# Performance work log

Hardware: AMD Instinct MI355X
Metric: run time of the kernel (lower is better)

The kernel has to match this reference:

```python
import jax, jax.numpy as jnp
import numpy as np

B, A, D, K = 128, 64, 256, 2048


def setup_inputs() -> dict:
    key = jax.random.key(0)
    k1, k2, k3, k4 = jax.random.split(key, 4)
    return {
        "continuous_latent": jax.random.normal(k1, (B, A, D), dtype=jnp.float32),
        "codebook": jax.random.normal(k2, (K, D), dtype=jnp.float32),
        "codebook_weights": jax.random.uniform(k3, (K,), dtype=jnp.float32),
        "rand_idx": jax.random.randint(k4, (K,), 0, B * A, dtype=jnp.int64)
        if jax.config.jax_enable_x64 else jax.random.randint(k4, (K,), 0, B * A, dtype=jnp.int32),
    }


def reference(continuous_latent, codebook, codebook_weights, rand_idx):
    b, a, d = continuous_latent.shape
    k = codebook.shape[0]
    sg = jax.lax.stop_gradient

    # (same math as the torch broadcast-subtract-square-sum, but avoids the
    # (B, A, K, D) intermediate by using a GEMM)
    x_sq = jnp.sum(continuous_latent * continuous_latent, axis=-1, keepdims=True)  # (B, A, 1)
    c_sq = jnp.sum(codebook * codebook, axis=-1)                                   # (K,)
    xc = jnp.einsum("bad,kd->bak", continuous_latent, codebook)                    # (B, A, K)
    distances = x_sq + c_sq[None, None, :] - 2.0 * xc                              # (B, A, K)

    soft_one_hot = jax.nn.softmax(-100.0 * distances, axis=-1)  # (B, A, K)

    args_selected = jnp.argmin(distances, axis=-1)  # (B, A)
    quantized = codebook[args_selected]             # (B, A, D)

    # Uselessness: pull rarely-used codes toward random encoder outputs.
    random_latents = continuous_latent.reshape(b * a, d)[rand_idx]  # (K, D)
    total_samples = jnp.sum(codebook_weights)
    unused = codebook_weights < total_samples / (100.0 * k)         # (K,)
    diff = jnp.where(unused[:, None], sg(random_latents) - codebook,
                     jnp.zeros_like(codebook))
    uselessness = jnp.mean(jnp.sum(jnp.log(jnp.abs(diff) + 1.0), axis=-1))

    quantization_loss = jnp.mean(
        jnp.sum((continuous_latent - quantized) ** 2, axis=-1))

    # Straight-through estimator
    quantized_ste = sg(quantized) + continuous_latent - sg(continuous_latent)

    # Latent diversity: mean over (B, B, A) of ||x_i,a - x_j,a||^2, computed
    # via the norm expansion to avoid the (B, B, A, D) intermediate.
    n = jnp.sum(continuous_latent * continuous_latent, axis=-1)         # (B, A)
    inner = jnp.einsum("iad,jad->ija", continuous_latent, continuous_latent)
    latent_diversity = jnp.mean(n[:, None, :] + n[None, :, :] - 2.0 * inner)

    probs = jnp.ones_like(quantized_ste[..., 0]) / k  # (B, A)

    return (quantized_ste, probs, soft_one_hot,
            quantization_loss, uselessness, latent_diversity)
```

## Files before the change

### kernel.cpp

```cpp
#include <hip/hip_runtime.h>

#define B_ 128
#define A_ 64
#define D_ 256
#define K_ 2048
#define R_ (B_*A_)
#define KEFF 512
#define QB 32

typedef __attribute__((ext_vector_type(8))) short bf16x8;
typedef __attribute__((ext_vector_type(4))) float f32x4;

__device__ inline float waveReduceSum(float v) {
    #pragma unroll
    for (int off = 32; off > 0; off >>= 1)
        v += __shfl_xor(v, off, 64);
    return v;
}
__device__ inline unsigned short f2bf(float f) {
    unsigned int u = __float_as_uint(f);
    return (unsigned short)((u + 0x7fffu + ((u >> 16) & 1u)) >> 16);
}
__device__ inline float bf2f(unsigned short h) {
    return __uint_as_float((unsigned int)h << 16);
}
__device__ inline bool ltidx(float a, int ia, float b, int ib) {
    return a < b || (a == b && ia < ib);
}

__global__ __launch_bounds__(256) void prologue_kernel(
        const float* __restrict__ X, const float* __restrict__ C,
        const float* __restrict__ W, const int* __restrict__ ridx,
        short* __restrict__ XPs, short* __restrict__ CP1s,
        float* __restrict__ xsq, float* __restrict__ csq,
        float* __restrict__ cspart, double* __restrict__ acc) {
    int bid = blockIdx.x;
    int wave = threadIdx.x >> 6, lane = threadIdx.x & 63;
    if (bid < 2048) {
        int row = bid * 4 + wave;
        int korig = lane * 4;
        float4 v = *reinterpret_cast<const float4*>(X + (size_t)row * D_ + korig);
        float f[4] = {v.x, v.y, v.z, v.w};
        ushort4 hi, lo;
        unsigned short* hp = (unsigned short*)&hi;
        unsigned short* lp = (unsigned short*)&lo;
        float s = 0.f;
        #pragma unroll
        for (int q = 0; q < 4; ++q) {
            s += f[q] * f[q];
            unsigned short h = f2bf(f[q]);
            hp[q] = h;
            lp[q] = f2bf(f[q] - bf2f(h));
        }
        int S = row >> 5, r32 = row & 31;
        int t = korig >> 5, kc = (korig >> 3) & 3, j = korig & 7;
        size_t base = (size_t)S * 16384 + (size_t)kc * 256 + (size_t)r32 * 8 + j;
        *reinterpret_cast<ushort4*>(XPs + base + (size_t)t * 1024)       = hi;
        *reinterpret_cast<ushort4*>(XPs + base + (size_t)(t + 8) * 1024) = lo;
        s = waveReduceSum(s);
        if (lane == 0) xsq[row] = s;
    } else if (bid < 2560) {
        int row = (bid - 2048) * 4 + wave;
        int korig = lane * 4;
        float4 v = *reinterpret_cast<const float4*>(C + (size_t)row * D_ + korig);
        float f[4] = {v.x, v.y, v.z, v.w};
        ushort4 hi, lo;
        unsigned short* hp = (unsigned short*)&hi;
        unsigned short* lp = (unsigned short*)&lo;
        float s = 0.f;
        #pragma unroll
        for (int q = 0; q < 4; ++q) {
            s += f[q] * f[q];
            unsigned short h = f2bf(f[q]);
            hp[q] = h;
            lp[q] = f2bf(f[q] - bf2f(h));
        }
        int rb = row >> 7, r = row & 127;
        int t = korig >> 5, kc = (korig >> 3) & 3, j = korig & 7;
        size_t base = ((size_t)rb * 16) * 4096 + (size_t)kc * 1024 + (size_t)r * 8 + j;
        *reinterpret_cast<ushort4*>(CP1s + base + (size_t)t * 4096)       = hi;
        *reinterpret_cast<ushort4*>(CP1s + base + (size_t)(t + 8) * 4096) = lo;
        s = waveReduceSum(s);
        if (lane == 0) csq[row] = s;
    } else if (bid < 2624) {
        int idx = (bid - 2560) * 256 + threadIdx.x;
        float s = 0.f;
        #pragma unroll 4
        for (int i = 0; i < B_; ++i) s += X[(size_t)i * (A_*D_) + idx];
        float p = s * s;
        p = waveReduceSum(p);
        __shared__ float red[4];
        if (lane == 0) red[wave] = p;
        __syncthreads();
        if (threadIdx.x == 0) cspart[bid - 2560] = red[0] + red[1] + red[2] + red[3];
    } else {
        double s = 0.0;
        for (int i = threadIdx.x; i < K_; i += 256) s += (double)W[i];
        __shared__ double red[256];
        red[threadIdx.x] = s; __syncthreads();
        for (int off = 128; off > 0; off >>= 1) {
            if (threadIdx.x < off) red[threadIdx.x] += red[threadIdx.x + off];
            __syncthreads();
        }
        float cutoff = (float)(red[0] / (100.0 * (double)K_));
        int k = (bid - 2624) * 4 + wave;
        if (!(W[k] < cutoff)) return;
        int r = ridx[k];
        float4 xv = *reinterpret_cast<const float4*>(X + (size_t)r * D_ + lane * 4);
        float4 cv = *reinterpret_cast<const float4*>(C + (size_t)k * D_ + lane * 4);
        float u = logf(fabsf(xv.x - cv.x) + 1.f) + logf(fabsf(xv.y - cv.y) + 1.f)
                + logf(fabsf(xv.z - cv.z) + 1.f) + logf(fabsf(xv.w - cv.w) + 1.f);
        u = waveReduceSum(u);
        if (lane == 0) atomicAdd(acc + 3, (double)u);
    }
}

__global__ __launch_bounds__(512, 2) void fused_dist_softmax(
        const short* __restrict__ XPs, const short* __restrict__ CP1s,
        const float* __restrict__ xsq, const float* __restrict__ csq,
        const float* __restrict__ X, const float* __restrict__ C,
        float* __restrict__ soft, float* __restrict__ outq,
        float* __restrict__ probs, float* __restrict__ qlrow) {
    __shared__ short ALDS[16384];
    __shared__ float csl[K_];
    __shared__ float xls[QB];
    __shared__ float4 wtop[8][QB];
    __shared__ float wsuml[8][QB];
    __shared__ float4 ffin[QB];
    __shared__ float finv[QB];

    int tid = threadIdx.x;
    int lane = tid & 63, w = tid >> 6;
    int S = blockIdx.x;
    int kc = lane >> 4, lr = lane & 15;

    #pragma unroll
    for (int p = 0; p < 4; ++p) {
        int seg0 = p * 16 + w * 2;
        const short* gsrc = XPs + (size_t)S * 16384
                          + (size_t)(seg0 + (lane >> 5)) * 256 + (lane & 31) * 8;
        short* ldst = &ALDS[seg0 * 256];
        __builtin_amdgcn_global_load_lds(
            (const __attribute__((address_space(1))) unsigned int*)gsrc,
            (__attribute__((address_space(3))) unsigned int*)ldst, 16, 0, 0);
    }
    *reinterpret_cast<float4*>(&csl[tid * 4]) =
        *reinterpret_cast<const float4*>(csq + tid * 4);
    if (tid < QB) xls[tid] = xsq[S * QB + tid];
    __syncthreads();

    f32x4 acc[2][16] = {};

    for (int tau = 0; tau < 16; ++tau) {
        const int ta = tau & 7;
        bf16x8 a1[2], a2[2];
        #pragma unroll
        for (int rt = 0; rt < 2; ++rt) {
            a1[rt] = *(const bf16x8*)(&ALDS[((ta * 4 + kc) * 32 + rt * 16 + lr) * 8]);
            a2[rt] = *(const bf16x8*)(&ALDS[(((ta + 8) * 4 + kc) * 32 + rt * 16 + lr) * 8]);
        }
        #pragma unroll
        for (int g = 0; g < 4; ++g) {
            const int cb = w * 2 + (g >> 1);
            const short* bbase = CP1s + ((size_t)(cb * 16 + tau)) * 4096
                               + (size_t)kc * 1024 + (size_t)lr * 8
                               + (size_t)((g & 1) * 4) * 128;
            bf16x8 bfr[4];
            #pragma unroll
            for (int c4 = 0; c4 < 4; ++c4)
                bfr[c4] = *(const bf16x8*)(bbase + c4 * 128);
            #pragma unroll
            for (int c4 = 0; c4 < 4; ++c4) {
                const int ct = g * 4 + c4;
                #pragma unroll
                for (int rt = 0; rt < 2; ++rt) {
                    acc[rt][ct] = __builtin_amdgcn_mfma_f32_16x16x32_bf16(bfr[c4], a1[rt], acc[rt][ct], 0, 0, 0);
                    acc[rt][ct] = __builtin_amdgcn_mfma_f32_16x16x32_bf16(bfr[c4], a2[rt], acc[rt][ct], 0, 0, 0);
                }
            }
        }
    }

    const float4* csl4 = reinterpret_cast<const float4*>(csl);

    #pragma unroll
    for (int rt = 0; rt < 2; ++rt) {
        int row32 = rt * 16 + lr;
        float xs = xls[row32];
        float bv1 = 3.4e38f, bv2 = 3.4e38f;
        int bi1 = 0x7fffffff, bi2 = 0x7fffffff;
        #pragma unroll
        for (int ct = 0; ct < 16; ++ct) {
            int col0 = w * 256 + ct * 16 + kc * 4;
            float4 cs = csl4[col0 >> 2];
            float csa[4] = {cs.x, cs.y, cs.z, cs.w};
            #pragma unroll
            for (int j = 0; j < 4; ++j) {
                float d = fmaf(-2.f, acc[rt][ct][j], xs + csa[j]);
                int idx = col0 + j;
                if (d < bv1) { bv2 = bv1; bi2 = bi1; bv1 = d; bi1 = idx; }
                else if (ltidx(d, idx, bv2, bi2)) { bv2 = d; bi2 = idx; }
            }
        }
        #pragma unroll
        for (int off = 16; off <= 32; off <<= 1) {
            float o1 = __shfl_xor(bv1, off, 64); int oi1 = __shfl_xor(bi1, off, 64);
            float o2 = __shfl_xor(bv2, off, 64); int oi2 = __shfl_xor(bi2, off, 64);
            if (ltidx(o1, oi1, bv1, bi1)) {
                if (ltidx(bv1, bi1, o2, oi2)) { bv2 = bv1; bi2 = bi1; }
                else                          { bv2 = o2;  bi2 = oi2; }
                bv1 = o1; bi1 = oi1;
            } else if (ltidx(o1, oi1, bv2, bi2)) { bv2 = o1; bi2 = oi1; }
        }
        if (kc == 0)
            wtop[w][row32] = make_float4(bv1, __int_as_float(bi1),
                                         bv2, __int_as_float(bi2));
    }
    __syncthreads();

    if (tid < QB) {
        float4 m = wtop[0][tid];
        float f1 = m.x; int a1i = __float_as_int(m.y);
        float f2 = m.z; int a2i = __float_as_int(m.w);
        #pragma unroll
        for (int ww = 1; ww < 8; ++ww) {
            float4 q = wtop[ww][tid];
            float o1 = q.x; int oi1 = __float_as_int(q.y);
            float o2 = q.z; int oi2 = __float_as_int(q.w);
            if (ltidx(o1, oi1, f1, a1i)) {
                if (ltidx(f1, a1i, o2, oi2)) { f2 = f1; a2i = a1i; }
                else                         { f2 = o2; a2i = oi2; }
                f1 = o1; a1i = oi1;
            } else if (ltidx(o1, oi1, f2, a2i)) { f2 = o1; a2i = oi1; }
        }
        ffin[tid] = make_float4(f1, __int_as_float(a1i), f2, __int_as_float(a2i));
    }
    __syncthreads();

    #pragma unroll
    for (int rt = 0; rt < 2; ++rt) {
        int row32 = rt * 16 + lr;
        float xs = xls[row32];
        float dm = ffin[row32].x;
        float psum = 0.f;
        #pragma unroll
        for (int ct = 0; ct < 16; ++ct) {
            int col0 = w * 256 + ct * 16 + kc * 4;
            float4 cs = csl4[col0 >> 2];
            float csa[4] = {cs.x, cs.y, cs.z, cs.w};
            #pragma unroll
            for (int j = 0; j < 4; ++j) {
                float d = fmaf(-2.f, acc[rt][ct][j], xs + csa[j]);
                float e = __expf(-100.f * (d - dm));
                acc[rt][ct][j] = e;
                psum += e;
            }
        }
        #pragma unroll
        for (int off = 16; off <= 32; off <<= 1) psum += __shfl_xor(psum, off, 64);
        if (kc == 0) wsuml[w][row32] = psum;
    }
    __syncthreads();
    if (tid < QB) {
        float s = 0.f;
        #pragma unroll
        for (int ww = 0; ww < 8; ++ww) s += wsuml[ww][tid];
        finv[tid] = 1.f / s;
    }
    __syncthreads();

    size_t rowbase = (size_t)S * QB;
    #pragma unroll
    for (int rt = 0; rt < 2; ++rt) {
        int row32 = rt * 16 + lr;
        float inv = finv[row32];
        float* dst0 = soft + (rowbase + row32) * K_ + w * 256 + kc * 4;
        #pragma unroll
        for (int ct = 0; ct < 16; ++ct) {
            f32x4 o = acc[rt][ct] * inv;
            *reinterpret_cast<f32x4*>(dst0 + ct * 16) = o;
        }
    }

    #pragma unroll
    for (int i = 0; i < 4; ++i) {
        int row32 = w * 4 + i;
        size_t grow = rowbase + row32;
        float4 fm = ffin[row32];
        int am = __float_as_int(fm.y), am2 = __float_as_int(fm.w);
        float4 x  = *reinterpret_cast<const float4*>(X + grow * D_ + lane * 4);
        float4 c1 = *reinterpret_cast<const float4*>(C + (size_t)am  * D_ + lane * 4);
        float4 c2 = *reinterpret_cast<const float4*>(C + (size_t)am2 * D_ + lane * 4);
        float d1 = (x.x-c1.x)*(x.x-c1.x) + (x.y-c1.y)*(x.y-c1.y)
                 + (x.z-c1.z)*(x.z-c1.z) + (x.w-c1.w)*(x.w-c1.w);
        float d2 = (x.x-c2.x)*(x.x-c2.x) + (x.y-c2.y)*(x.y-c2.y)
                 + (x.z-c2.z)*(x.z-c2.z) + (x.w-c2.w)*(x.w-c2.w);
        d1 = waveReduceSum(d1);
        d2 = waveReduceSum(d2);
        bool p2 = ltidx(d2, am2, d1, am);
        float4 q = p2 ? c2 : c1;
        *reinterpret_cast<float4*>(outq + grow * D_ + lane * 4) = q;
        if (lane == 0) {
            qlrow[grow] = p2 ? d2 : d1;
            probs[grow] = 1.0f / (float)K_;
        }
    }
}

__global__ void row_sqnorm(const float* __restrict__ X, float* __restrict__ out, int rows) {
    int wave = threadIdx.x >> 6, lane = threadIdx.x & 63;
    int row  = blockIdx.x * 4 + wave;
    if (row >= rows) return;
    float4 v = *reinterpret_cast<const float4*>(X + (size_t)row * D_ + lane * 4);
    float s = v.x*v.x + v.y*v.y + v.z*v.z + v.w*v.w;
    s = waveReduceSum(s);
    if (lane == 0) out[row] = s;
}

__global__ void col_sum_sq(const float* __restrict__ X, float* __restrict__ part) {
    int idx = blockIdx.x * blockDim.x + threadIdx.x;
    float s = 0.f;
    #pragma unroll 4
    for (int i = 0; i < B_; ++i) s += X[(size_t)i * (A_*D_) + idx];
    float p = s * s;
    p = waveReduceSum(p);
    __shared__ float red[4];
    int wave = threadIdx.x >> 6, lane = threadIdx.x & 63;
    if (lane == 0) red[wave] = p;
    __syncthreads();
    if (threadIdx.x == 0) part[blockIdx.x] = red[0] + red[1] + red[2] + red[3];
}

__global__ void wsum_kernel(const float* __restrict__ w, double* __restrict__ acc) {
    double s = 0.0;
    for (int i = threadIdx.x; i < K_; i += 256) s += (double)w[i];
    __shared__ double red[256];
    red[threadIdx.x] = s; __syncthreads();
    for (int off = 128; off > 0; off >>= 1) {
        if (threadIdx.x < off) red[threadIdx.x] += red[threadIdx.x + off];
        __syncthreads();
    }
    if (threadIdx.x == 0) acc[2] = red[0];
}

__global__ void useless_kernel(const float* __restrict__ X, const float* __restrict__ C,
                               const float* __restrict__ w, const int* __restrict__ ridx,
                               const double* __restrict__ acc_in, double* __restrict__ use_acc) {
    int wave = threadIdx.x >> 6, lane = threadIdx.x & 63;
    int k = blockIdx.x * 4 + wave;
    if (k >= K_) return;
    float cutoff = (float)(acc_in[2] / (100.0 * (double)K_));
    if (!(w[k] < cutoff)) return;
    int r = ridx[k];
    float4 xv = *reinterpret_cast<const float4*>(X + (size_t)r * D_ + lane * 4);
    float4 cv = *reinterpret_cast<const float4*>(C + (size_t)k * D_ + lane * 4);
    float s = logf(fabsf(xv.x - cv.x) + 1.f) + logf(fabsf(xv.y - cv.y) + 1.f)
            + logf(fabsf(xv.z - cv.z) + 1.f) + logf(fabsf(xv.w - cv.w) + 1.f);
    s = waveReduceSum(s);
    if (lane == 0) atomicAdd(use_acc, (double)s);
}

#define BM 128
#define BN 128
#define BK 16
__global__ __launch_bounds__(256, 4) void dist_gemm(
        const float* __restrict__ X, const float* __restrict__ C,
        const float* __restrict__ xsq, const float* __restrict__ csq,
        float* __restrict__ Dist) {
    __shared__ float As[BK][BM + 4];
    __shared__ float Bs[BK][BN + 4];
    int tid = threadIdx.x;
    int tx = tid & 15, ty = tid >> 4;
    int bm0 = blockIdx.y * BM, bn0 = blockIdx.x * BN;
    int r = tid & 127;
    const float* src = (tid < 128) ? (X + (size_t)(bm0 + r) * D_)
                                   : (C + (size_t)(bn0 + r) * D_);
    float* dst = (tid < 128) ? &As[0][0] : &Bs[0][0];
    float acc[2][2][4][4] = {};
    float4 p0 = *reinterpret_cast<const float4*>(src + 0);
    float4 p1 = *reinterpret_cast<const float4*>(src + 4);
    float4 p2 = *reinterpret_cast<const float4*>(src + 8);
    float4 p3 = *reinterpret_cast<const float4*>(src + 12);
    for (int t = 0; t < D_ / BK; ++t) {
        __syncthreads();
        dst[ 0*(BM+4) + r] = p0.x; dst[ 1*(BM+4) + r] = p0.y;
        dst[ 2*(BM+4) + r] = p0.z; dst[ 3*(BM+4) + r] = p0.w;
        dst[ 4*(BM+4) + r] = p1.x; dst[ 5*(BM+4) + r] = p1.y;
        dst[ 6*(BM+4) + r] = p1.z; dst[ 7*(BM+4) + r] = p1.w;
        dst[ 8*(BM+4) + r] = p2.x; dst[ 9*(BM+4) + r] = p2.y;
        dst[10*(BM+4) + r] = p2.z; dst[11*(BM+4) + r] = p2.w;
        dst[12*(BM+4) + r] = p3.x; dst[13*(BM+4) + r] = p3.y;
        dst[14*(BM+4) + r] = p3.z; dst[15*(BM+4) + r] = p3.w;
        __syncthreads();
        if (t < D_ / BK - 1) {
            const float* s2 = src + (t + 1) * BK;
            p0 = *reinterpret_cast<const float4*>(s2 + 0);
            p1 = *reinterpret_cast<const float4*>(s2 + 4);
            p2 = *reinterpret_cast<const float4*>(s2 + 8);
            p3 = *reinterpret_cast<const float4*>(s2 + 12);
        }
        #pragma unroll
        for (int kk = 0; kk < BK; ++kk) {
            float4 a0 = *reinterpret_cast<const float4*>(&As[kk][ty * 4]);
            float4 a1 = *reinterpret_cast<const float4*>(&As[kk][64 + ty * 4]);
            float4 b0 = *reinterpret_cast<const float4*>(&Bs[kk][tx * 4]);
            float4 b1 = *reinterpret_cast<const float4*>(&Bs[kk][64 + tx * 4]);
            float af[2][4] = {{a0.x, a0.y, a0.z, a0.w}, {a1.x, a1.y, a1.z, a1.w}};
            float bf[2][4] = {{b0.x, b0.y, b0.z, b0.w}, {b1.x, b1.y, b1.z, b1.w}};
            #pragma unroll
            for (int rg = 0; rg < 2; ++rg)
                #pragma unroll
                for (int cg = 0; cg < 2; ++cg)
                    #pragma unroll
                    for (int i = 0; i < 4; ++i)
                        #pragma unroll
                        for (int j = 0; j < 4; ++j)
                            acc[rg][cg][i][j] += af[rg][i] * bf[cg][j];
        }
    }
    #pragma unroll
    for (int rg = 0; rg < 2; ++rg)
        #pragma unroll
        for (int i = 0; i < 4; ++i) {
            int row = bm0 + rg * 64 + ty * 4 + i;
            float xs = xsq[row];
            #pragma unroll
            for (int cg = 0; cg < 2; ++cg) {
                int col = bn0 + cg * 64 + tx * 4;
                float4 cs = *reinterpret_cast<const float4*>(csq + col);
                float4 o;
                o.x = xs + cs.x - 2.f * acc[rg][cg][i][0];
                o.y = xs + cs.y - 2.f * acc[rg][cg][i][1];
                o.z = xs + cs.z - 2.f * acc[rg][cg][i][2];
                o.w = xs + cs.w - 2.f * acc[rg][cg][i][3];
                *reinterpret_cast<float4*>(Dist + (size_t)row * K_ + col) = o;
            }
        }
}

__global__ __launch_bounds__(256) void softmax_quant(
        float* __restrict__ Dist, const float* __restrict__ X,
        const float* __restrict__ C, float* __restrict__ outq,
        float* __restrict__ probs, float* __restrict__ qlrow) {
    int row = blockIdx.x;
    int t = threadIdx.x;
    int wave = t >> 6, lane = t & 63;
    float* drow = Dist + (size_t)row * K_;

    float v[8];
    float4 v0 = *reinterpret_cast<const float4*>(drow + t * 8);
    float4 v1v = *reinterpret_cast<const float4*>(drow + t * 8 + 4);
    v[0]=v0.x; v[1]=v0.y; v[2]=v0.z; v[3]=v0.w;
    v[4]=v1v.x; v[5]=v1v.y; v[6]=v1v.z; v[7]=v1v.w;

    float v1 = v[0]; int i1 = t * 8;
    float v2 = 3.4e38f; int i2 = 0x7fffffff;
    #pragma unroll
    for (int j = 1; j < 8; ++j) {
        int idx = t * 8 + j;
        if (v[j] < v1) { v2 = v1; i2 = i1; v1 = v[j]; i1 = idx; }
        else if (ltidx(v[j], idx, v2, i2)) { v2 = v[j]; i2 = idx; }
    }
    #pragma unroll
    for (int off = 32; off > 0; off >>= 1) {
        float w1 = __shfl_xor(v1, off, 64); int j1 = __shfl_xor(i1, off, 64);
        float w2 = __shfl_xor(v2, off, 64); int j2 = __shfl_xor(i2, off, 64);
        if (ltidx(w1, j1, v1, i1)) {
            if (ltidx(v1, i1, w2, j2)) { v2 = v1; i2 = i1; }
            else                       { v2 = w2; i2 = j2; }
            v1 = w1; i1 = j1;
        } else if (ltidx(w1, j1, v2, i2)) { v2 = w1; i2 = j1; }
    }
    __shared__ float sv1[4], sv2[4]; __shared__ int si1[4], si2[4];
    __shared__ float ws[4];
    if (lane == 0) { sv1[wave] = v1; si1[wave] = i1; sv2[wave] = v2; si2[wave] = i2; }
    __syncthreads();
    float dmin = sv1[0]; int am = si1[0];
    float d2nd = sv2[0]; int am2 = si2[0];
    #pragma unroll
    for (int w = 1; w < 4; ++w) {
        float w1 = sv1[w]; int j1 = si1[w];
        float w2 = sv2[w]; int j2 = si2[w];
        if (ltidx(w1, j1, dmin, am)) {
            if (ltidx(dmin, am, w2, j2)) { d2nd = dmin; am2 = am; }
            else                         { d2nd = w2;   am2 = j2; }
            dmin = w1; am = j1;
        } else if (ltidx(w1, j1, d2nd, am2)) { d2nd = w1; am2 = j1; }
    }

    float e[8]; float s = 0.f;
    #pragma unroll
    for (int j = 0; j < 8; ++j) { e[j] = __expf(-100.f * (v[j] - dmin)); s += e[j]; }
    s = waveReduceSum(s);
    if (lane == 0) ws[wave] = s;
    __syncthreads();
    float inv = 1.f / (ws[0] + ws[1] + ws[2] + ws[3]);

    float4 o0 = make_float4(e[0]*inv, e[1]*inv, e[2]*inv, e[3]*inv);
    float4 o1 = make_float4(e[4]*inv, e[5]*inv, e[6]*inv, e[7]*inv);
    *reinterpret_cast<float4*>(drow + t * 8)     = o0;
    *reinterpret_cast<float4*>(drow + t * 8 + 4) = o1;

    if (wave == 0) {
        float4 x  = *reinterpret_cast<const float4*>(X + (size_t)row * D_ + lane * 4);
        float4 c1 = *reinterpret_cast<const float4*>(C + (size_t)am  * D_ + lane * 4);
        float4 c2 = *reinterpret_cast<const float4*>(C + (size_t)am2 * D_ + lane * 4);
        float d1x = (x.x-c1.x)*(x.x-c1.x) + (x.y-c1.y)*(x.y-c1.y)
                  + (x.z-c1.z)*(x.z-c1.z) + (x.w-c1.w)*(x.w-c1.w);
        float d2x = (x.x-c2.x)*(x.x-c2.x) + (x.y-c2.y)*(x.y-c2.y)
                  + (x.z-c2.z)*(x.z-c2.z) + (x.w-c2.w)*(x.w-c2.w);
        d1x = waveReduceSum(d1x);
        d2x = waveReduceSum(d2x);
        bool pick2 = ltidx(d2x, am2, d1x, am);
        float4 q = pick2 ? c2 : c1;
        float dq = pick2 ? d2x : d1x;
        *reinterpret_cast<float4*>(outq + (size_t)row * D_ + lane * 4) = q;
        if (lane == 0) {
            qlrow[row] = dq;
            probs[row] = 1.0f / (float)K_;
        }
    }
}

__global__ __launch_bounds__(256) void finalize_kernel(
        const double* __restrict__ acc, const float* __restrict__ xsq,
        const float* __restrict__ qlrow, const float* __restrict__ cspart,
        float* __restrict__ o) {
    int t = threadIdx.x;
    double xs = 0.0, ql = 0.0, cs = 0.0;
    for (int i = t; i < R_; i += 256) { xs += (double)xsq[i]; ql += (double)qlrow[i]; }
    if (t < 64) cs = (double)cspart[t];
    __shared__ double r0[256], r1[256], r2[256];
    r0[t] = xs; r1[t] = ql; r2[t] = cs;
    __syncthreads();
    for (int off = 128; off > 0; off >>= 1) {
        if (t < off) { r0[t] += r0[t+off]; r1[t] += r1[t+off]; r2[t] += r2[t+off]; }
        __syncthreads();
    }
    if (t == 0) {
        o[0] = (float)(r1[0] / (double)R_);
        o[1] = (float)(acc[3] / (double)K_);
        o[2] = (float)(2.0 * r0[0] / (double)R_
                     - 2.0 * r2[0] / ((double)B_ * (double)B_ * (double)A_));
    }
}

extern "C" void kernel_launch(void* const* d_in, const int* in_sizes, int n_in,
                              void* d_out, int out_size, void* d_ws, size_t ws_size,
                              hipStream_t stream) {
    const float* X  = (const float*)d_in[0];
    const float* C  = (const float*)d_in[1];
    const float* W  = (const float*)d_in[2];
    const int*   RI = (const int*)d_in[3];

    float* out    = (float*)d_out;
    float* out_q  = out;
    float* out_p  = out_q + (size_t)R_ * D_;
    float* out_s  = out_p + R_;
    float* out_sc = out_s + (size_t)R_ * K_;

    char* wsb = (char*)d_ws;
    double* acc   = (double*)wsb;
    float*  xsq   = (float*)(wsb + 64);
    float*  csq   = (float*)(wsb + 64 + R_*4);
    float*  qlrow = (float*)(wsb + 64 + R_*4 + K_*4);
    float*  cspart= (float*)(wsb + 64 + R_*4 + K_*4 + R_*4);
    short*  CP1s  = (short*)(wsb + 64 + R_*4 + K_*4 + R_*4 + 256);

    const size_t WS_NEEDED = 64 + (size_t)R_*4 + (size_t)K_*4 + (size_t)R_*4 + 256
                           + (size_t)K_*KEFF*2;

    hipMemsetAsync(d_ws, 0, 64, stream);

    if (ws_size >= WS_NEEDED) {
        short* XPs = (short*)out_q;
        hipLaunchKernelGGL(prologue_kernel, dim3(3136), dim3(256), 0, stream,
                           X, C, W, RI, XPs, CP1s, xsq, csq, cspart, acc);
        hipLaunchKernelGGL(fused_dist_softmax, dim3(R_/QB), dim3(512), 0, stream,
                           XPs, CP1s, xsq, csq, X, C, out_s, out_q, out_p, qlrow);
    } else {
        hipLaunchKernelGGL(row_sqnorm, dim3(R_/4), dim3(256), 0, stream, X, xsq, R_);
        hipLaunchKernelGGL(row_sqnorm, dim3(K_/4), dim3(256), 0, stream, C, csq, K_);
        hipLaunchKernelGGL(col_sum_sq, dim3((A_*D_)/256), dim3(256), 0, stream, X, cspart);
        hipLaunchKernelGGL(wsum_kernel, dim3(1), dim3(256), 0, stream, W, acc);
        hipLaunchKernelGGL(useless_kernel, dim3(K_/4), dim3(256), 0, stream,
                           X, C, W, RI, acc, acc + 3);
        hipLaunchKernelGGL(dist_gemm, dim3(K_/BN, R_/BM), dim3(256), 0, stream, X, C, xsq, csq, out_s);
        hipLaunchKernelGGL(softmax_quant, dim3(R_), dim3(256), 0, stream, out_s, X, C, out_q, out_p, qlrow);
    }

    hipLaunchKernelGGL(finalize_kernel, dim3(1), dim3(256), 0, stream, acc, xsq, qlrow, cspart, out_sc);
}
```

Before: 89.70 us.

## Fuse X bf16 hi/lo split and row norms into the distance kernel

Moves the conversion of X into split bf16 hi/lo fragments, and its row-norm computation, from the prologue kernel into the fused distance/softmax kernel. Each block now writes its A tile straight into LDS and xsq to global, so the XPs scratch round-trip and 2048 prologue blocks go away. The K loop is reordered to reuse the A fragments for both tau halves, and distances are kept in the accumulators so the softmax pass does not recompute them. The cost is extra per-block conversion work and higher register pressure before the GEMM.

```diff
diff --git a/kernel.cpp b/kernel.cpp
--- a/kernel.cpp
+++ b/kernel.cpp
@@ -31,36 +31,12 @@
 __global__ __launch_bounds__(256) void prologue_kernel(
         const float* __restrict__ X, const float* __restrict__ C,
         const float* __restrict__ W, const int* __restrict__ ridx,
-        short* __restrict__ XPs, short* __restrict__ CP1s,
-        float* __restrict__ xsq, float* __restrict__ csq,
+        short* __restrict__ CP1s, float* __restrict__ csq,
         float* __restrict__ cspart, double* __restrict__ acc) {
     int bid = blockIdx.x;
     int wave = threadIdx.x >> 6, lane = threadIdx.x & 63;
-    if (bid < 2048) {
+    if (bid < 512) {
         int row = bid * 4 + wave;
-        int korig = lane * 4;
-        float4 v = *reinterpret_cast<const float4*>(X + (size_t)row * D_ + korig);
-        float f[4] = {v.x, v.y, v.z, v.w};
-        ushort4 hi, lo;
-        unsigned short* hp = (unsigned short*)&hi;
-        unsigned short* lp = (unsigned short*)&lo;
-        float s = 0.f;
-        #pragma unroll
-        for (int q = 0; q < 4; ++q) {
-            s += f[q] * f[q];
-            unsigned short h = f2bf(f[q]);
-            hp[q] = h;
-            lp[q] = f2bf(f[q] - bf2f(h));
-        }
-        int S = row >> 5, r32 = row & 31;
-        int t = korig >> 5, kc = (korig >> 3) & 3, j = korig & 7;
-        size_t base = (size_t)S * 16384 + (size_t)kc * 256 + (size_t)r32 * 8 + j;
-        *reinterpret_cast<ushort4*>(XPs + base + (size_t)t * 1024)       = hi;
-        *reinterpret_cast<ushort4*>(XPs + base + (size_t)(t + 8) * 1024) = lo;
-        s = waveReduceSum(s);
-        if (lane == 0) xsq[row] = s;
-    } else if (bid < 2560) {
-        int row = (bid - 2048) * 4 + wave;
         int korig = lane * 4;
         float4 v = *reinterpret_cast<const float4*>(C + (size_t)row * D_ + korig);
         float f[4] = {v.x, v.y, v.z, v.w};
@@ -82,8 +58,8 @@
         *reinterpret_cast<ushort4*>(CP1s + base + (size_t)(t + 8) * 4096) = lo;
         s = waveReduceSum(s);
         if (lane == 0) csq[row] = s;
-    } else if (bid < 2624) {
-        int idx = (bid - 2560) * 256 + threadIdx.x;
+    } else if (bid < 576) {
+        int idx = (bid - 512) * 256 + threadIdx.x;
         float s = 0.f;
         #pragma unroll 4
         for (int i = 0; i < B_; ++i) s += X[(size_t)i * (A_*D_) + idx];
@@ -92,7 +68,7 @@
         __shared__ float red[4];
         if (lane == 0) red[wave] = p;
         __syncthreads();
-        if (threadIdx.x == 0) cspart[bid - 2560] = red[0] + red[1] + red[2] + red[3];
+        if (threadIdx.x == 0) cspart[bid - 512] = red[0] + red[1] + red[2] + red[3];
     } else {
         double s = 0.0;
         for (int i = threadIdx.x; i < K_; i += 256) s += (double)W[i];
@@ -103,7 +79,7 @@
             __syncthreads();
         }
         float cutoff = (float)(red[0] / (100.0 * (double)K_));
-        int k = (bid - 2624) * 4 + wave;
+        int k = (bid - 576) * 4 + wave;
         if (!(W[k] < cutoff)) return;
         int r = ridx[k];
         float4 xv = *reinterpret_cast<const float4*>(X + (size_t)r * D_ + lane * 4);
@@ -116,11 +92,11 @@
 }
 
 __global__ __launch_bounds__(512, 2) void fused_dist_softmax(
-        const short* __restrict__ XPs, const short* __restrict__ CP1s,
-        const float* __restrict__ xsq, const float* __restrict__ csq,
+        const short* __restrict__ CP1s, const float* __restrict__ csq,
         const float* __restrict__ X, const float* __restrict__ C,
-        float* __restrict__ soft, float* __restrict__ outq,
-        float* __restrict__ probs, float* __restrict__ qlrow) {
+        float* __restrict__ xsq, float* __restrict__ soft,
+        float* __restrict__ outq, float* __restrict__ probs,
+        float* __restrict__ qlrow) {
     __shared__ short ALDS[16384];
     __shared__ float csl[K_];
     __shared__ float xls[QB];
@@ -134,25 +110,45 @@
     int S = blockIdx.x;
     int kc = lane >> 4, lr = lane & 15;
 
-    #pragma unroll
-    for (int p = 0; p < 4; ++p) {
-        int seg0 = p * 16 + w * 2;
-        const short* gsrc = XPs + (size_t)S * 16384
-                          + (size_t)(seg0 + (lane >> 5)) * 256 + (lane & 31) * 8;
-        short* ldst = &ALDS[seg0 * 256];
-        __builtin_amdgcn_global_load_lds(
-            (const __attribute__((address_space(1))) unsigned int*)gsrc,
-            (__attribute__((address_space(3))) unsigned int*)ldst, 16, 0, 0);
-    }
     *reinterpret_cast<float4*>(&csl[tid * 4]) =
         *reinterpret_cast<const float4*>(csq + tid * 4);
-    if (tid < QB) xls[tid] = xsq[S * QB + tid];
+
+    {
+        int r32 = tid >> 4;
+        int c0 = (tid & 15) * 16;
+        const float* xrow = X + ((size_t)S * QB + r32) * D_ + c0;
+        float ssq = 0.f;
+        #pragma unroll
+        for (int i = 0; i < 4; ++i) {
+            float4 v = *reinterpret_cast<const float4*>(xrow + 4 * i);
+            float f[4] = {v.x, v.y, v.z, v.w};
+            ushort4 hi, lo;
+            unsigned short* hp = (unsigned short*)&hi;
+            unsigned short* lp = (unsigned short*)&lo;
+            #pragma unroll
+            for (int q = 0; q < 4; ++q) {
+                ssq += f[q] * f[q];
+                unsigned short h = f2bf(f[q]);
+                hp[q] = h;
+                lp[q] = f2bf(f[q] - bf2f(h));
+            }
+            int korig = c0 + 4 * i;
+            int tt = korig >> 5, kcc = (korig >> 3) & 3, j = korig & 7;
+            *reinterpret_cast<ushort4*>(&ALDS[(((tt    ) * 4 + kcc) * 32 + r32) * 8 + j]) = hi;
+            *reinterpret_cast<ushort4*>(&ALDS[(((tt + 8) * 4 + kcc) * 32 + r32) * 8 + j]) = lo;
+        }
+        #pragma unroll
+        for (int off = 1; off <= 8; off <<= 1) ssq += __shfl_xor(ssq, off, 64);
+        if ((lane & 15) == 0) {
+            xls[r32] = ssq;
+            xsq[(size_t)S * QB + r32] = ssq;
+        }
+    }
     __syncthreads();
 
     f32x4 acc[2][16] = {};
 
-    for (int tau = 0; tau < 16; ++tau) {
-        const int ta = tau & 7;
+    for (int ta = 0; ta < 8; ++ta) {
         bf16x8 a1[2], a2[2];
         #pragma unroll
         for (int rt = 0; rt < 2; ++rt) {
@@ -160,22 +156,26 @@
             a2[rt] = *(const bf16x8*)(&ALDS[(((ta + 8) * 4 + kc) * 32 + rt * 16 + lr) * 8]);
         }
         #pragma unroll
-        for (int g = 0; g < 4; ++g) {
-            const int cb = w * 2 + (g >> 1);
-            const short* bbase = CP1s + ((size_t)(cb * 16 + tau)) * 4096
-                               + (size_t)kc * 1024 + (size_t)lr * 8
-                               + (size_t)((g & 1) * 4) * 128;
-            bf16x8 bfr[4];
+        for (int tt = 0; tt < 2; ++tt) {
+            const int tau = ta + tt * 8;
             #pragma unroll
-            for (int c4 = 0; c4 < 4; ++c4)
-                bfr[c4] = *(const bf16x8*)(bbase + c4 * 128);
-            #pragma unroll
-            for (int c4 = 0; c4 < 4; ++c4) {
-                const int ct = g * 4 + c4;
+            for (int g = 0; g < 4; ++g) {
+                const int cb = w * 2 + (g >> 1);
+                const short* bbase = CP1s + ((size_t)(cb * 16 + tau)) * 4096
+                                   + (size_t)kc * 1024 + (size_t)lr * 8
+                                   + (size_t)((g & 1) * 4) * 128;
+                bf16x8 bfr[4];
                 #pragma unroll
-                for (int rt = 0; rt < 2; ++rt) {
-                    acc[rt][ct] = __builtin_amdgcn_mfma_f32_16x16x32_bf16(bfr[c4], a1[rt], acc[rt][ct], 0, 0, 0);
-                    acc[rt][ct] = __builtin_amdgcn_mfma_f32_16x16x32_bf16(bfr[c4], a2[rt], acc[rt][ct], 0, 0, 0);
+                for (int c4 = 0; c4 < 4; ++c4)
+                    bfr[c4] = *(const bf16x8*)(bbase + c4 * 128);
+                #pragma unroll
+                for (int c4 = 0; c4 < 4; ++c4) {
+                    const int ct = g * 4 + c4;
+                    #pragma unroll
+                    for (int rt = 0; rt < 2; ++rt) {
+                        acc[rt][ct] = __builtin_amdgcn_mfma_f32_16x16x32_bf16(bfr[c4], a1[rt], acc[rt][ct], 0, 0, 0);
+                        acc[rt][ct] = __builtin_amdgcn_mfma_f32_16x16x32_bf16(bfr[c4], a2[rt], acc[rt][ct], 0, 0, 0);
+                    }
                 }
             }
         }
@@ -197,6 +197,7 @@
             #pragma unroll
             for (int j = 0; j < 4; ++j) {
                 float d = fmaf(-2.f, acc[rt][ct][j], xs + csa[j]);
+                acc[rt][ct][j] = d;
                 int idx = col0 + j;
                 if (d < bv1) { bv2 = bv1; bi2 = bi1; bv1 = d; bi1 = idx; }
                 else if (ltidx(d, idx, bv2, bi2)) { bv2 = d; bi2 = idx; }
@@ -240,18 +241,13 @@
     #pragma unroll
     for (int rt = 0; rt < 2; ++rt) {
         int row32 = rt * 16 + lr;
-        float xs = xls[row32];
         float dm = ffin[row32].x;
         float psum = 0.f;
         #pragma unroll
         for (int ct = 0; ct < 16; ++ct) {
-            int col0 = w * 256 + ct * 16 + kc * 4;
-            float4 cs = csl4[col0 >> 2];
-            float csa[4] = {cs.x, cs.y, cs.z, cs.w};
             #pragma unroll
             for (int j = 0; j < 4; ++j) {
-                float d = fmaf(-2.f, acc[rt][ct][j], xs + csa[j]);
-                float e = __expf(-100.f * (d - dm));
+                float e = __expf(-100.f * (acc[rt][ct][j] - dm));
                 acc[rt][ct][j] = e;
                 psum += e;
             }
@@ -573,11 +569,10 @@
     hipMemsetAsync(d_ws, 0, 64, stream);
 
     if (ws_size >= WS_NEEDED) {
-        short* XPs = (short*)out_q;
-        hipLaunchKernelGGL(prologue_kernel, dim3(3136), dim3(256), 0, stream,
-                           X, C, W, RI, XPs, CP1s, xsq, csq, cspart, acc);
+        hipLaunchKernelGGL(prologue_kernel, dim3(1088), dim3(256), 0, stream,
+                           X, C, W, RI, CP1s, csq, cspart, acc);
         hipLaunchKernelGGL(fused_dist_softmax, dim3(R_/QB), dim3(512), 0, stream,
-                           XPs, CP1s, xsq, csq, X, C, out_s, out_q, out_p, qlrow);
+                           CP1s, csq, X, C, xsq, out_s, out_q, out_p, qlrow);
     } else {
         hipLaunchKernelGGL(row_sqnorm, dim3(R_/4), dim3(256), 0, stream, X, xsq, R_);
         hipLaunchKernelGGL(row_sqnorm, dim3(K_/4), dim3(256), 0, stream, C, csq, K_);
```

Measured after the change: 87.41 us. -2.6%, faster.
